# Kernel tuning notes

Measured on AMD Instinct MI355X. Metric: run time of the kernel, lower is better.

The kernel has to match this reference:

```python
import jax, jax.numpy as jnp
import numpy as np

K = 9        # 3x3 kernel -> kernel*kernel
KSIZE = 3
GROUP = 1


def setup_inputs() -> dict:
    key = jax.random.key(0)
    k1, k2 = jax.random.split(key)
    N, C, H, W = 8, 640, 48, 48
    query = jax.random.normal(k1, (N, C, H, W), dtype=jnp.float32)
    # [N, H*W, K, 1]: reshape(-1, K) yields rows ordered (n, h*w) as the bmm expects
    dynamic_filter = jax.random.normal(k2, (N, H * W, K, 1), dtype=jnp.float32)
    return {"query": query, "dynamic_filter": dynamic_filter}


def reference(query, dynamic_filter):
    N, C, H, W = query.shape
    Nf, Cf, Hf, Wf = dynamic_filter.shape
    # nn.Unfold(kernel=3, padding=1, dilation=1): pad then gather 3x3 shifted views.
    xp = jnp.pad(query, ((0, 0), (0, 0), (1, 1), (1, 1)))
    # patches: [N, C, K, H, W]; kernel offsets row-major, matching torch unfold's
    # [N, C*K, L] layout viewed as (N, C, K, H*W).
    patches = jnp.stack(
        [xp[:, :, i:i + H, j:j + W] for i in range(KSIZE) for j in range(KSIZE)],
        axis=2,
    )
    # dynamic_filter.reshape(-1, K) with our [N, H*W, K, 1] layout == per-pixel K-vector.
    df = dynamic_filter.reshape(N, H, W, K)
    # bmm over batch (n, h*w): contract the K (tap) axis per channel, per pixel.
    out = jnp.einsum('nckhw,nhwk->nchw', patches, df)
    out1 = jax.nn.relu(out)
    return out1, jnp.zeros((Nf, Cf, Hf, Wf), dtype=query.dtype)
```

## Files before the change

### kernel.cpp

```cpp
#include <hip/hip_runtime.h>

#define N_   8
#define C_   640
#define H_   48
#define W_   48
#define K_   9
#define CH   16
#define NCC  (C_ / CH)
#define BLK  256
#define HB   3
#define NBLK (N_ * NCC * HB)
#define OUT1_ELEMS ((size_t)N_ * C_ * H_ * W_)
#define OUT2_ELEMS ((size_t)N_ * H_ * W_ * K_)

typedef float f4 __attribute__((ext_vector_type(4)));

__global__ __launch_bounds__(BLK, 4) void dynconv(
    const float* __restrict__ q,
    const float* __restrict__ df,
    float* __restrict__ out)
{
    const int tid = threadIdx.x;
    const int bid = blockIdx.x;
    const int swz = (bid & 7) * (NBLK / 8) + (bid >> 3);

    {
        size_t g = (size_t)bid * BLK + tid;
        if (g < OUT2_ELEMS) out[OUT1_ELEMS + g] = 0.f;
    }

    const int p     = tid & 15;
    const int rowid = tid >> 4;
    if (p >= 12) return;

    const int hb = swz % HB;
    const int cc = (swz / HB) % NCC;
    const int n  = swz / (HB * NCC);
    const int h  = hb * 16 + rowid;
    const int w0 = p * 4;
    const int c0 = cc * CH;

    const f4* dfp = (const f4*)(df + (size_t)(n * (H_ * W_) + h * W_ + w0) * K_);
    f4 t0 = dfp[0], t1 = dfp[1], t2 = dfp[2], t3 = dfp[3], t4 = dfp[4],
       t5 = dfp[5], t6 = dfp[6], t7 = dfp[7], t8 = dfp[8];

    int roff[3];
#pragma unroll
    for (int dy = 0; dy < 3; ++dy) {
        int r  = h + dy - 1;
        int rc = min(max(r, 0), H_ - 1);
        roff[dy] = (rc - h) * W_;
    }

    const size_t plane = (size_t)H_ * W_;
    const float* qbase = q   + ((size_t)(n * C_ + c0)) * plane + h * W_ + w0;
    float*       obase = out + ((size_t)(n * C_ + c0)) * plane + h * W_ + w0;

    f4 m0[3], m1[3];
#pragma unroll
    for (int dy = 0; dy < 3; ++dy) m0[dy] = *(const f4*)(qbase + roff[dy]);
    {
        const float* qp = qbase + plane;
#pragma unroll
        for (int dy = 0; dy < 3; ++dy) m1[dy] = *(const f4*)(qp + roff[dy]);
    }

    float f[36];
    f[ 0]=t0.x; f[ 1]=t0.y; f[ 2]=t0.z; f[ 3]=t0.w;
    f[ 4]=t1.x; f[ 5]=t1.y; f[ 6]=t1.z; f[ 7]=t1.w;
    f[ 8]=t2.x; f[ 9]=t2.y; f[10]=t2.z; f[11]=t2.w;
    f[12]=t3.x; f[13]=t3.y; f[14]=t3.z; f[15]=t3.w;
    f[16]=t4.x; f[17]=t4.y; f[18]=t4.z; f[19]=t4.w;
    f[20]=t5.x; f[21]=t5.y; f[22]=t5.z; f[23]=t5.w;
    f[24]=t6.x; f[25]=t6.y; f[26]=t6.z; f[27]=t6.w;
    f[28]=t7.x; f[29]=t7.y; f[30]=t7.z; f[31]=t7.w;
    f[32]=t8.x; f[33]=t8.y; f[34]=t8.z; f[35]=t8.w;

    const float tm = (h == 0)      ? 0.f : 1.f;
    const float bm = (h == H_ - 1) ? 0.f : 1.f;
    const float lm = (p == 0)      ? 0.f : 1.f;
    const float rm = (p == 11)     ? 0.f : 1.f;
#pragma unroll
    for (int px = 0; px < 4; ++px) {
        f[px*9+0] *= tm; f[px*9+1] *= tm; f[px*9+2] *= tm;
        f[px*9+6] *= bm; f[px*9+7] *= bm; f[px*9+8] *= bm;
    }
    f[ 0] *= lm; f[ 3] *= lm; f[ 6] *= lm;
    f[29] *= rm; f[32] *= rm; f[35] *= rm;

#pragma unroll
    for (int ci = 0; ci < CH; ++ci) {
        asm volatile("" : "+v"(m0[0]), "+v"(m0[1]), "+v"(m0[2]));

        float lft[3], rgt[3];
#pragma unroll
        for (int dy = 0; dy < 3; ++dy) {
            lft[dy] = __shfl_up(m0[dy].w, 1);
            rgt[dy] = __shfl_down(m0[dy].x, 1);
        }

        f4 acc = (f4){0.f, 0.f, 0.f, 0.f};
#pragma unroll
        for (int dy = 0; dy < 3; ++dy) {
            const int fb = dy * 3;
            const f4 m = m0[dy];
            acc.x = fmaf(f[ 0 + fb], lft[dy], acc.x);
            acc.x = fmaf(f[ 1 + fb], m.x,     acc.x);
            acc.x = fmaf(f[ 2 + fb], m.y,     acc.x);

            acc.y = fmaf(f[ 9 + fb], m.x,     acc.y);
            acc.y = fmaf(f[10 + fb], m.y,     acc.y);
            acc.y = fmaf(f[11 + fb], m.z,     acc.y);

            acc.z = fmaf(f[18 + fb], m.y,     acc.z);
            acc.z = fmaf(f[19 + fb], m.z,     acc.z);
            acc.z = fmaf(f[20 + fb], m.w,     acc.z);

            acc.w = fmaf(f[27 + fb], m.z,     acc.w);
            acc.w = fmaf(f[28 + fb], m.w,     acc.w);
            acc.w = fmaf(f[29 + fb], rgt[dy], acc.w);
        }
        acc.x = fmaxf(acc.x, 0.f);
        acc.y = fmaxf(acc.y, 0.f);
        acc.z = fmaxf(acc.z, 0.f);
        acc.w = fmaxf(acc.w, 0.f);
        *(f4*)(obase + (size_t)ci * plane) = acc;

        if (ci + 1 < CH) {
#pragma unroll
            for (int dy = 0; dy < 3; ++dy) m0[dy] = m1[dy];
            if (ci + 2 < CH) {
                const float* qp = qbase + (size_t)(ci + 2) * plane;
#pragma unroll
                for (int dy = 0; dy < 3; ++dy) m1[dy] = *(const f4*)(qp + roff[dy]);
            }
        }
    }
}

extern "C" void kernel_launch(void* const* d_in, const int* in_sizes, int n_in,
                              void* d_out, int out_size, void* d_ws, size_t ws_size,
                              hipStream_t stream)
{
    const float* q  = (const float*)d_in[0];
    const float* df = (const float*)d_in[1];
    float* out = (float*)d_out;

    dynconv<<<NBLK, BLK, 0, stream>>>(q, df, out);
}
```

Measured before the change: 21.36 us.

## Stage dynamic filter through LDS with coalesced loads and deepen prefetch

The per-pixel filter taps for the block's 16 rows are now loaded cooperatively by all 256 threads in contiguous f4 chunks, stored to shared memory, and each thread then reads its 9 f4 taps from LDS. Before, each thread did strided 9×f4 loads straight from global memory. The query row prefetch also goes from double to triple buffering. The change is meant to improve coalescing of the filter loads and hide more global load latency. In exchange it adds a block-wide barrier, about 27 KB of LDS per block (which may limit occupancy), and more registers.

```diff
diff --git a/kernel.cpp b/kernel.cpp
--- a/kernel.cpp
+++ b/kernel.cpp
@@ -10,6 +10,7 @@
 #define BLK  256
 #define HB   3
 #define NBLK (N_ * NCC * HB)
+#define DF_F4   1728
 #define OUT1_ELEMS ((size_t)N_ * C_ * H_ * W_)
 #define OUT2_ELEMS ((size_t)N_ * H_ * W_ * K_)
 
@@ -20,6 +21,8 @@
     const float* __restrict__ df,
     float* __restrict__ out)
 {
+    __shared__ f4 sdf[DF_F4];
+
     const int tid = threadIdx.x;
     const int bid = blockIdx.x;
     const int swz = (bid & 7) * (NBLK / 8) + (bid >> 3);
@@ -31,7 +34,6 @@
 
     const int p     = tid & 15;
     const int rowid = tid >> 4;
-    if (p >= 12) return;
 
     const int hb = swz % HB;
     const int cc = (swz / HB) % NCC;
@@ -40,9 +42,14 @@
     const int w0 = p * 4;
     const int c0 = cc * CH;
 
-    const f4* dfp = (const f4*)(df + (size_t)(n * (H_ * W_) + h * W_ + w0) * K_);
-    f4 t0 = dfp[0], t1 = dfp[1], t2 = dfp[2], t3 = dfp[3], t4 = dfp[4],
-       t5 = dfp[5], t6 = dfp[6], t7 = dfp[7], t8 = dfp[8];
+    const f4* dfg = (const f4*)(df + (size_t)n * (H_ * W_ * K_)
+                                   + (size_t)hb * 16 * W_ * K_);
+    f4 stg[7];
+#pragma unroll
+    for (int i = 0; i < 7; ++i) {
+        int idx = tid + i * BLK;
+        if (idx < DF_F4) stg[i] = dfg[idx];
+    }
 
     int roff[3];
 #pragma unroll
@@ -56,25 +63,36 @@
     const float* qbase = q   + ((size_t)(n * C_ + c0)) * plane + h * W_ + w0;
     float*       obase = out + ((size_t)(n * C_ + c0)) * plane + h * W_ + w0;
 
-    f4 m0[3], m1[3];
+    f4 m0[3], m1[3], m2[3];
+    if (p < 12) {
 #pragma unroll
-    for (int dy = 0; dy < 3; ++dy) m0[dy] = *(const f4*)(qbase + roff[dy]);
-    {
-        const float* qp = qbase + plane;
+        for (int dy = 0; dy < 3; ++dy) m0[dy] = *(const f4*)(qbase + roff[dy]);
+        const float* qp1 = qbase + plane;
 #pragma unroll
-        for (int dy = 0; dy < 3; ++dy) m1[dy] = *(const f4*)(qp + roff[dy]);
+        for (int dy = 0; dy < 3; ++dy) m1[dy] = *(const f4*)(qp1 + roff[dy]);
+        const float* qp2 = qbase + 2 * plane;
+#pragma unroll
+        for (int dy = 0; dy < 3; ++dy) m2[dy] = *(const f4*)(qp2 + roff[dy]);
     }
 
+#pragma unroll
+    for (int i = 0; i < 7; ++i) {
+        int idx = tid + i * BLK;
+        if (idx < DF_F4) sdf[idx] = stg[i];
+    }
+    __syncthreads();
+
+    if (p >= 12) return;
+
     float f[36];
-    f[ 0]=t0.x; f[ 1]=t0.y; f[ 2]=t0.z; f[ 3]=t0.w;
-    f[ 4]=t1.x; f[ 5]=t1.y; f[ 6]=t1.z; f[ 7]=t1.w;
-    f[ 8]=t2.x; f[ 9]=t2.y; f[10]=t2.z; f[11]=t2.w;
-    f[12]=t3.x; f[13]=t3.y; f[14]=t3.z; f[15]=t3.w;
-    f[16]=t4.x; f[17]=t4.y; f[18]=t4.z; f[19]=t4.w;
-    f[20]=t5.x; f[21]=t5.y; f[22]=t5.z; f[23]=t5.w;
-    f[24]=t6.x; f[25]=t6.y; f[26]=t6.z; f[27]=t6.w;
-    f[28]=t7.x; f[29]=t7.y; f[30]=t7.z; f[31]=t7.w;
-    f[32]=t8.x; f[33]=t8.y; f[34]=t8.z; f[35]=t8.w;
+    {
+        const f4* tp = &sdf[rowid * 108 + p * 9];
+#pragma unroll
+        for (int i = 0; i < 9; ++i) {
+            f4 v = tp[i];
+            f[4*i+0] = v.x; f[4*i+1] = v.y; f[4*i+2] = v.z; f[4*i+3] = v.w;
+        }
+    }
 
     const float tm = (h == 0)      ? 0.f : 1.f;
     const float bm = (h == H_ - 1) ? 0.f : 1.f;
@@ -128,11 +146,11 @@
 
         if (ci + 1 < CH) {
 #pragma unroll
-            for (int dy = 0; dy < 3; ++dy) m0[dy] = m1[dy];
-            if (ci + 2 < CH) {
-                const float* qp = qbase + (size_t)(ci + 2) * plane;
+            for (int dy = 0; dy < 3; ++dy) { m0[dy] = m1[dy]; m1[dy] = m2[dy]; }
+            if (ci + 3 < CH) {
+                const float* qp = qbase + (size_t)(ci + 3) * plane;
 #pragma unroll
-                for (int dy = 0; dy < 3; ++dy) m1[dy] = *(const f4*)(qp + roff[dy]);
+                for (int dy = 0; dy < 3; ++dy) m2[dy] = *(const f4*)(qp + roff[dy]);
             }
         }
     }
```

After: 20.50 us. 4.0% less time.
